# Kernel tuning notes

Measured on AMD Instinct MI355X. Metric: run time of the kernel, lower is better.

Reference implementation:

```python
import jax, jax.numpy as jnp
import numpy as np

N = 12000
E = 384000
NEG_SLOPE = 0.2


def add_self_loops(edge_index, n):
    loops = jnp.arange(n, dtype=edge_index.dtype)
    return jnp.concatenate([edge_index, jnp.stack([loops, loops])], axis=1)


def gat_conv(x, edge_index, W, a_src, a_dst, b, n):
    # PyG GATConv, heads=1, concat=True, add_self_loops=True
    h = x @ W                      # [N, F_out]
    ei = add_self_loops(edge_index, n)
    src, dst = ei[0], ei[1]
    alpha_s = h @ a_src            # [N]
    alpha_d = h @ a_dst            # [N]
    e = jax.nn.leaky_relu(alpha_s[src] + alpha_d[dst], NEG_SLOPE)  # [E+N]
    # segment softmax over incoming edges of each dst node
    m = jax.ops.segment_max(e, dst, num_segments=n)
    ex = jnp.exp(e - m[dst])
    s = jax.ops.segment_sum(ex, dst, num_segments=n)
    alpha = ex / s[dst]
    out = jax.ops.segment_sum(alpha[:, None] * h[src], dst, num_segments=n)
    return out + b


def setup_inputs() -> dict:
    key = jax.random.key(0)
    ks = jax.random.split(key, 10)
    x = jax.random.normal(ks[0], (N, 40), dtype=jnp.float32)
    edge_index = jax.random.randint(ks[1], (2, E), 0, N, dtype=jnp.int64)
    sc1 = 1.0 / np.sqrt(40.0)
    sc2 = 1.0 / np.sqrt(50.0)
    return {
        "x": x,
        "edge_index": edge_index,
        "W1": jax.random.normal(ks[2], (40, 50), dtype=jnp.float32) * sc1,
        "a_src1": jax.random.normal(ks[3], (50,), dtype=jnp.float32) * sc2,
        "a_dst1": jax.random.normal(ks[4], (50,), dtype=jnp.float32) * sc2,
        "b1": jnp.zeros((50,), dtype=jnp.float32),
        "W2": jax.random.normal(ks[5], (50, 40), dtype=jnp.float32) * sc2,
        "a_src2": jax.random.normal(ks[6], (40,), dtype=jnp.float32) * sc1,
        "a_dst2": jax.random.normal(ks[7], (40,), dtype=jnp.float32) * sc1,
        "b2": jnp.zeros((40,), dtype=jnp.float32),
    }


def reference(x, edge_index, W1, a_src1, a_dst1, b1, W2, a_src2, a_dst2, b2):
    h = jax.nn.relu(gat_conv(x, edge_index, W1, a_src1, a_dst1, b1, N))
    z = jax.nn.relu(gat_conv(h, edge_index, W2, a_src2, a_dst2, b2, N))
    adj_pred = jax.nn.sigmoid(z @ z.T)   # [N, N] inner-product decoder
    return adj_pred
```

## Files before the change

### kernel.cpp

```cpp
#include <hip/hip_runtime.h>
#include <cstdint>
#include <cstddef>

#define N_NODES 12000
#define N_EDGES 384000
#define NEG_SLOPE 0.2f

__device__ __forceinline__ float leaky(float v) { return v > 0.f ? v : NEG_SLOPE * v; }

template <int FIN, int FOUT>
__global__ __launch_bounds__(256) void node_linear(
    const float* __restrict__ x, const float* __restrict__ W,
    const float* __restrict__ a_src, const float* __restrict__ a_dst,
    float* __restrict__ h, float* __restrict__ as_, float* __restrict__ ad_) {
  __shared__ float Ws[FIN * FOUT];
  __shared__ float av[FOUT], dv[FOUT];
  for (int i = threadIdx.x; i < FIN * FOUT; i += blockDim.x) Ws[i] = W[i];
  if (threadIdx.x < FOUT) {
    av[threadIdx.x] = a_src[threadIdx.x];
    dv[threadIdx.x] = a_dst[threadIdx.x];
  }
  __syncthreads();
  const int node = blockIdx.x * blockDim.x + threadIdx.x;
  if (node >= N_NODES) return;
  float xr[FIN];
#pragma unroll
  for (int k = 0; k < FIN; ++k) xr[k] = x[node * FIN + k];
  float ssum = 0.f, dsum = 0.f;
#pragma unroll 1
  for (int c = 0; c < FOUT; ++c) {
    float acc = 0.f;
#pragma unroll
    for (int k = 0; k < FIN; ++k) acc += xr[k] * Ws[k * FOUT + c];
    h[node * FOUT + c] = acc;
    ssum += acc * av[c];
    dsum += acc * dv[c];
  }
  as_[node] = ssum;
  ad_[node] = dsum;
}

__global__ __launch_bounds__(256) void histo_kernel(const int* __restrict__ dst,
                                                    int* __restrict__ deg) {
  const int i = blockIdx.x * blockDim.x + threadIdx.x;
  if (i >= N_EDGES + N_NODES) return;
  const int d = (i < N_EDGES) ? dst[i] : (i - N_EDGES);
  atomicAdd(&deg[d], 1);
}

__global__ __launch_bounds__(1024) void scan_kernel(const int* __restrict__ deg,
                                                    int* __restrict__ rowp) {
  __shared__ int sm[1024];
  __shared__ int carry;
  const int t = threadIdx.x;
  if (t == 0) carry = 0;
  __syncthreads();
  for (int base = 0; base < N_NODES; base += 1024) {
    const int idx = base + t;
    const int v = (idx < N_NODES) ? deg[idx] : 0;
    sm[t] = v;
    __syncthreads();
    int run = v;
    for (int off = 1; off < 1024; off <<= 1) {
      const int other = (t >= off) ? sm[t - off] : 0;
      __syncthreads();
      run += other;
      sm[t] = run;
      __syncthreads();
    }
    const int c = carry;
    if (idx < N_NODES) rowp[idx] = c + run - v;
    __syncthreads();
    if (t == 1023) carry = c + run;
    __syncthreads();
  }
  if (t == 0) rowp[N_NODES] = carry;
}

__global__ __launch_bounds__(256) void scatter_kernel(
    const int* __restrict__ src, const int* __restrict__ dst,
    const int* __restrict__ rowp, int* __restrict__ fill,
    int* __restrict__ esrc) {
  const int i = blockIdx.x * blockDim.x + threadIdx.x;
  if (i >= N_EDGES + N_NODES) return;
  int s, d;
  if (i < N_EDGES) {
    s = src[i];
    d = dst[i];
  } else {
    s = d = i - N_EDGES;
  }
  const int pos = rowp[d] + atomicAdd(&fill[d], 1);
  esrc[pos] = s;
}

template <int F>
__global__ __launch_bounds__(256) void gat_aggregate(
    const int* __restrict__ rowp, const int* __restrict__ esrc,
    const float* __restrict__ h, const float* __restrict__ as_,
    const float* __restrict__ ad_, const float* __restrict__ b,
    float* __restrict__ out) {
  const int wid = (blockIdx.x * blockDim.x + threadIdx.x) >> 6;
  const int lane = threadIdx.x & 63;
  if (wid >= N_NODES) return;
  const int start = rowp[wid], end = rowp[wid + 1];
  const float adv = ad_[wid];

  float m = -1e30f;
  for (int i = start + lane; i < end; i += 64) m = fmaxf(m, leaky(as_[esrc[i]] + adv));
#pragma unroll
  for (int off = 32; off > 0; off >>= 1) m = fmaxf(m, __shfl_xor(m, off));

  float ssum = 0.f;
  for (int i = start + lane; i < end; i += 64) ssum += __expf(leaky(as_[esrc[i]] + adv) - m);
#pragma unroll
  for (int off = 32; off > 0; off >>= 1) ssum += __shfl_xor(ssum, off);
  const float inv = 1.0f / ssum;

  float acc = 0.f;
  for (int i = start; i < end; ++i) {
    const int s = esrc[i];
    const float w = __expf(leaky(as_[s] + adv) - m);
    if (lane < F) acc += w * h[s * F + lane];
  }
  if (lane < F) {
    const float o = acc * inv + b[lane];
    out[wid * F + lane] = o > 0.f ? o : 0.f;
  }
}

__global__ __launch_bounds__(256) void decoder_kernel(const float* __restrict__ z,
                                                      float* __restrict__ out) {
  __shared__ float At[40][132];
  __shared__ float Bt[40][132];
  const int i0 = blockIdx.y * 128;
  const int j0 = blockIdx.x * 128;
  const int t = threadIdx.x;

  for (int u = t; u < 1280; u += 256) {
    const int row = u / 10;
    const int kq = u - row * 10;
    int ga = i0 + row;
    ga = ga < N_NODES ? ga : N_NODES - 1;
    const float4 va = *(const float4*)(z + ga * 40 + kq * 4);
    At[kq * 4 + 0][row] = va.x;
    At[kq * 4 + 1][row] = va.y;
    At[kq * 4 + 2][row] = va.z;
    At[kq * 4 + 3][row] = va.w;
    int gb = j0 + row;
    gb = gb < N_NODES ? gb : N_NODES - 1;
    const float4 vb = *(const float4*)(z + gb * 40 + kq * 4);
    Bt[kq * 4 + 0][row] = vb.x;
    Bt[kq * 4 + 1][row] = vb.y;
    Bt[kq * 4 + 2][row] = vb.z;
    Bt[kq * 4 + 3][row] = vb.w;
  }
  __syncthreads();

  const int tx = t & 15, ty = t >> 4;
  float acc[8][8] = {};
  for (int k = 0; k < 40; ++k) {
    float a[8], b[8];
    *(float4*)&a[0] = *(const float4*)&At[k][ty * 8];
    *(float4*)&a[4] = *(const float4*)&At[k][ty * 8 + 4];
    *(float4*)&b[0] = *(const float4*)&Bt[k][tx * 8];
    *(float4*)&b[4] = *(const float4*)&Bt[k][tx * 8 + 4];
#pragma unroll
    for (int r = 0; r < 8; ++r)
#pragma unroll
      for (int c = 0; c < 8; ++c) acc[r][c] += a[r] * b[c];
  }

#pragma unroll
  for (int r = 0; r < 8; ++r) {
    const int gi = i0 + ty * 8 + r;
    if (gi < N_NODES) {
      float o[8];
#pragma unroll
      for (int c = 0; c < 8; ++c) o[c] = 1.0f / (1.0f + __expf(-acc[r][c]));
      const int gj = j0 + tx * 8;
      float* dstp = out + (size_t)gi * N_NODES + gj;
      if (gj + 7 < N_NODES) {
        *(float4*)dstp = make_float4(o[0], o[1], o[2], o[3]);
        *(float4*)(dstp + 4) = make_float4(o[4], o[5], o[6], o[7]);
      } else {
#pragma unroll
        for (int c = 0; c < 8; ++c)
          if (gj + c < N_NODES) dstp[c] = o[c];
      }
    }
  }
}

extern "C" void kernel_launch(void* const* d_in, const int* in_sizes, int n_in,
                              void* d_out, int out_size, void* d_ws, size_t ws_size,
                              hipStream_t stream) {
  const float* x     = (const float*)d_in[0];
  const int*   ei    = (const int*)d_in[1];
  const float* W1    = (const float*)d_in[2];
  const float* asrc1 = (const float*)d_in[3];
  const float* adst1 = (const float*)d_in[4];
  const float* b1    = (const float*)d_in[5];
  const float* W2    = (const float*)d_in[6];
  const float* asrc2 = (const float*)d_in[7];
  const float* adst2 = (const float*)d_in[8];
  const float* b2    = (const float*)d_in[9];
  float* out = (float*)d_out;

  float* ws   = (float*)d_ws;
  float* h1   = ws;
  float* out1 = h1 + 600000;
  float* h2   = out1 + 600000;
  float* z    = h2 + 480000;
  float* as_  = z + 480000;
  float* ad_  = as_ + 12000;
  int* deg  = (int*)(ad_ + 12000);
  int* rowp = deg + 12000;
  int* fill = rowp + 12001;
  int* esrc = fill + 12000;

  const int* src = ei;
  const int* dst = ei + N_EDGES;

  hipMemsetAsync(deg, 0, N_NODES * sizeof(int), stream);
  hipMemsetAsync(fill, 0, N_NODES * sizeof(int), stream);

  const int eb = (N_EDGES + N_NODES + 255) / 256;
  histo_kernel<<<eb, 256, 0, stream>>>(dst, deg);
  scan_kernel<<<1, 1024, 0, stream>>>(deg, rowp);
  scatter_kernel<<<eb, 256, 0, stream>>>(src, dst, rowp, fill, esrc);

  const int nb = (N_NODES + 255) / 256;
  node_linear<40, 50><<<nb, 256, 0, stream>>>(x, W1, asrc1, adst1, h1, as_, ad_);
  gat_aggregate<50><<<3000, 256, 0, stream>>>(rowp, esrc, h1, as_, ad_, b1, out1);
  node_linear<50, 40><<<nb, 256, 0, stream>>>(out1, W2, asrc2, adst2, h2, as_, ad_);
  gat_aggregate<40><<<3000, 256, 0, stream>>>(rowp, esrc, h2, as_, ad_, b2, z);

  dim3 dgrid(94, 94);
  decoder_kernel<<<dgrid, 256, 0, stream>>>(z, out);
}
```

Before: 860.3 us.

## Exploit decoder symmetry, cache edge weights in aggregate, shuffle-based scan, merge memsets

```diff
diff --git a/kernel.cpp b/kernel.cpp
--- a/kernel.cpp
+++ b/kernel.cpp
@@ -50,31 +50,42 @@
 
 __global__ __launch_bounds__(1024) void scan_kernel(const int* __restrict__ deg,
                                                     int* __restrict__ rowp) {
-  __shared__ int sm[1024];
-  __shared__ int carry;
+  __shared__ int wsum[16];
+  __shared__ int carry_s;
   const int t = threadIdx.x;
-  if (t == 0) carry = 0;
+  const int lane = t & 63;
+  const int w = t >> 6;
+  if (t == 0) carry_s = 0;
   __syncthreads();
   for (int base = 0; base < N_NODES; base += 1024) {
     const int idx = base + t;
     const int v = (idx < N_NODES) ? deg[idx] : 0;
-    sm[t] = v;
+    int run = v;
+#pragma unroll
+    for (int off = 1; off < 64; off <<= 1) {
+      const int u = __shfl_up(run, off);
+      if (lane >= off) run += u;
+    }
+    if (lane == 63) wsum[w] = run;
     __syncthreads();
-    int run = v;
-    for (int off = 1; off < 1024; off <<= 1) {
-      const int other = (t >= off) ? sm[t - off] : 0;
-      __syncthreads();
-      run += other;
-      sm[t] = run;
-      __syncthreads();
-    }
-    const int c = carry;
-    if (idx < N_NODES) rowp[idx] = c + run - v;
+    if (w == 0) {
+      int x = (lane < 16) ? wsum[lane] : 0;
+#pragma unroll
+      for (int off = 1; off < 16; off <<= 1) {
+        const int u = __shfl_up(x, off);
+        if (lane >= off) x += u;
+      }
+      if (lane < 16) wsum[lane] = x;
+    }
     __syncthreads();
-    if (t == 1023) carry = c + run;
+    const int wpre = (w == 0) ? 0 : wsum[w - 1];
+    const int c = carry_s;
+    if (idx < N_NODES) rowp[idx] = c + wpre + run - v;
     __syncthreads();
-  }
-  if (t == 0) rowp[N_NODES] = carry;
+    if (t == 1023) carry_s = c + wsum[15];
+    __syncthreads();
+  }
+  if (t == 0) rowp[N_NODES] = carry_s;
 }
 
 __global__ __launch_bounds__(256) void scatter_kernel(
@@ -100,41 +111,73 @@
     const float* __restrict__ h, const float* __restrict__ as_,
     const float* __restrict__ ad_, const float* __restrict__ b,
     float* __restrict__ out) {
+  __shared__ float wc[4][128];
+  __shared__ int sc[4][128];
+  const int ws = threadIdx.x >> 6;
   const int wid = (blockIdx.x * blockDim.x + threadIdx.x) >> 6;
   const int lane = threadIdx.x & 63;
   if (wid >= N_NODES) return;
   const int start = rowp[wid], end = rowp[wid + 1];
   const float adv = ad_[wid];
 
-  float m = -1e30f;
-  for (int i = start + lane; i < end; i += 64) m = fmaxf(m, leaky(as_[esrc[i]] + adv));
-#pragma unroll
-  for (int off = 32; off > 0; off >>= 1) m = fmaxf(m, __shfl_xor(m, off));
-
-  float ssum = 0.f;
-  for (int i = start + lane; i < end; i += 64) ssum += __expf(leaky(as_[esrc[i]] + adv) - m);
-#pragma unroll
-  for (int off = 32; off > 0; off >>= 1) ssum += __shfl_xor(ssum, off);
-  const float inv = 1.0f / ssum;
-
-  float acc = 0.f;
-  for (int i = start; i < end; ++i) {
+  int s0 = 0, s1 = 0;
+  float e0 = -1e30f, e1 = -1e30f;
+  const int i0 = start + lane, i1 = start + 64 + lane;
+  if (i0 < end) { s0 = esrc[i0]; e0 = leaky(as_[s0] + adv); }
+  if (i1 < end) { s1 = esrc[i1]; e1 = leaky(as_[s1] + adv); }
+  float m = fmaxf(e0, e1);
+  for (int i = start + 128 + lane; i < end; i += 64)
+    m = fmaxf(m, leaky(as_[esrc[i]] + adv));
+#pragma unroll
+  for (int off = 32; off; off >>= 1) m = fmaxf(m, __shfl_xor(m, off));
+
+  const float w0 = (i0 < end) ? __expf(e0 - m) : 0.f;
+  const float w1 = (i1 < end) ? __expf(e1 - m) : 0.f;
+  float ssum = w0 + w1;
+  for (int i = start + 128 + lane; i < end; i += 64)
+    ssum += __expf(leaky(as_[esrc[i]] + adv) - m);
+#pragma unroll
+  for (int off = 32; off; off >>= 1) ssum += __shfl_xor(ssum, off);
+  const float inv = 1.f / ssum;
+
+  sc[ws][lane] = s0;
+  sc[ws][lane + 64] = s1;
+  wc[ws][lane] = w0;
+  wc[ws][lane + 64] = w1;
+
+  const int deg = end - start;
+  const int ncached = deg < 128 ? deg : 128;
+  float acc = 0.f, acc2 = 0.f;
+  int j = 0;
+  for (; j + 1 < ncached; j += 2) {
+    const int t0 = sc[ws][j], t1 = sc[ws][j + 1];
+    const float u0 = wc[ws][j], u1 = wc[ws][j + 1];
+    if (lane < F) {
+      acc += u0 * h[t0 * F + lane];
+      acc2 += u1 * h[t1 * F + lane];
+    }
+  }
+  for (; j < ncached; ++j)
+    if (lane < F) acc += wc[ws][j] * h[sc[ws][j] * F + lane];
+  for (int i = start + 128; i < end; ++i) {
     const int s = esrc[i];
     const float w = __expf(leaky(as_[s] + adv) - m);
     if (lane < F) acc += w * h[s * F + lane];
   }
   if (lane < F) {
-    const float o = acc * inv + b[lane];
+    const float o = (acc + acc2) * inv + b[lane];
     out[wid * F + lane] = o > 0.f ? o : 0.f;
   }
 }
 
 __global__ __launch_bounds__(256) void decoder_kernel(const float* __restrict__ z,
                                                       float* __restrict__ out) {
+  const int bx = blockIdx.x, by = blockIdx.y;
+  if (bx > by) return;
   __shared__ float At[40][132];
   __shared__ float Bt[40][132];
-  const int i0 = blockIdx.y * 128;
-  const int j0 = blockIdx.x * 128;
+  const int i0 = by * 128;
+  const int j0 = bx * 128;
   const int t = threadIdx.x;
 
   for (int u = t; u < 1280; u += 256) {
@@ -172,21 +215,40 @@
   }
 
 #pragma unroll
+  for (int r = 0; r < 8; ++r)
+#pragma unroll
+    for (int c = 0; c < 8; ++c) acc[r][c] = 1.0f / (1.0f + __expf(-acc[r][c]));
+
+#pragma unroll
   for (int r = 0; r < 8; ++r) {
     const int gi = i0 + ty * 8 + r;
     if (gi < N_NODES) {
-      float o[8];
-#pragma unroll
-      for (int c = 0; c < 8; ++c) o[c] = 1.0f / (1.0f + __expf(-acc[r][c]));
       const int gj = j0 + tx * 8;
       float* dstp = out + (size_t)gi * N_NODES + gj;
       if (gj + 7 < N_NODES) {
-        *(float4*)dstp = make_float4(o[0], o[1], o[2], o[3]);
-        *(float4*)(dstp + 4) = make_float4(o[4], o[5], o[6], o[7]);
+        *(float4*)dstp = make_float4(acc[r][0], acc[r][1], acc[r][2], acc[r][3]);
+        *(float4*)(dstp + 4) = make_float4(acc[r][4], acc[r][5], acc[r][6], acc[r][7]);
       } else {
 #pragma unroll
         for (int c = 0; c < 8; ++c)
-          if (gj + c < N_NODES) dstp[c] = o[c];
+          if (gj + c < N_NODES) dstp[c] = acc[r][c];
+      }
+    }
+  }
+
+  if (bx < by) {
+#pragma unroll
+    for (int c = 0; c < 8; ++c) {
+      const int gr = j0 + tx * 8 + c;
+      const int ci = i0 + ty * 8;
+      float* dstp = out + (size_t)gr * N_NODES + ci;
+      if (ci + 7 < N_NODES) {
+        *(float4*)dstp = make_float4(acc[0][c], acc[1][c], acc[2][c], acc[3][c]);
+        *(float4*)(dstp + 4) = make_float4(acc[4][c], acc[5][c], acc[6][c], acc[7][c]);
+      } else {
+#pragma unroll
+        for (int r = 0; r < 8; ++r)
+          if (ci + r < N_NODES) dstp[r] = acc[r][c];
       }
     }
   }
@@ -207,23 +269,22 @@
   const float* b2    = (const float*)d_in[9];
   float* out = (float*)d_out;
 
-  float* ws   = (float*)d_ws;
-  float* h1   = ws;
+  float* wsp  = (float*)d_ws;
+  float* h1   = wsp;
   float* out1 = h1 + 600000;
   float* h2   = out1 + 600000;
   float* z    = h2 + 480000;
   float* as_  = z + 480000;
   float* ad_  = as_ + 12000;
   int* deg  = (int*)(ad_ + 12000);
-  int* rowp = deg + 12000;
-  int* fill = rowp + 12001;
-  int* esrc = fill + 12000;
+  int* fill = deg + 12000;
+  int* rowp = fill + 12000;
+  int* esrc = rowp + 12001;
 
   const int* src = ei;
   const int* dst = ei + N_EDGES;
 
-  hipMemsetAsync(deg, 0, N_NODES * sizeof(int), stream);
-  hipMemsetAsync(fill, 0, N_NODES * sizeof(int), stream);
+  hipMemsetAsync(deg, 0, 2 * N_NODES * sizeof(int), stream);
 
   const int eb = (N_EDGES + N_NODES + 255) / 256;
   histo_kernel<<<eb, 256, 0, stream>>>(dst, deg);
```

Measured after the change: 793.7 us. 7.7% less time.
